# Kernel tuning notes

Hardware: AMD Instinct MI355X
Metric: run time of the kernel (lower is better)

The kernel has to match this reference:

```python
import jax, jax.numpy as jnp
import numpy as np

D = 1024       # d_model
L = 4          # num_layers
T = 2048       # sequence length


def setup_inputs() -> dict:
    key = jax.random.key(0)
    ks = jax.random.split(key, 8)
    lim = 1.0 / np.sqrt(2 * D)              # torch default Linear init bound
    xav = np.sqrt(6.0 / (2 * D + D))        # xavier_uniform for time_a/time_b
    u = lambda k, lo, hi: jax.random.uniform(k, (L, 2 * D, D), jnp.float32, lo, hi)
    return {
        "spatial_states": jax.random.normal(ks[0], (T, D), jnp.float32),
        "re_norm": jnp.float32(0.5),
        "dt_phys": jnp.float32(1.0),
        "re_proj_w": jax.random.uniform(ks[1], (D,), jnp.float32, -1.0, 1.0),  # Linear(1,D) weight, bound=1
        "re_proj_b": jax.random.uniform(ks[2], (D,), jnp.float32, -1.0, 1.0),
        "Wf1": u(ks[3], -lim, lim),
        "bf1": jnp.zeros((L, D), jnp.float32),
        "Wf2": u(ks[4], -lim, lim),
        "bf2": jnp.zeros((L, D), jnp.float32),
        "Wta": u(ks[5], -xav, xav),
        "bta": jnp.zeros((L, D), jnp.float32),
        "Wtb": u(ks[6], -xav, xav),
        "btb": jnp.zeros((L, D), jnp.float32),
    }


def reference(spatial_states, re_norm, dt_phys, re_proj_w, re_proj_b,
              Wf1, bf1, Wf2, bf2, Wta, bta, Wtb, btb):
    d = re_proj_w.shape[0]
    # persistent Re residual bias added to every timestep
    seq = spatial_states + re_norm * re_proj_w + re_proj_b  # [T, D]
    n_layers = Wf1.shape[0]
    for l in range(n_layers):
        # fuse the 4 per-cell linears into one [2D, 4D] GEMV per step
        W = jnp.concatenate([Wf1[l], Wf2[l], Wta[l], Wtb[l]], axis=1)  # [2D, 4D]
        b = jnp.concatenate([bf1[l], bf2[l], bta[l], btb[l]])          # [4D]

        def step(h, x, W=W, b=b):
            xh = jnp.concatenate([x, h])          # [2D]
            z = xh @ W + b                        # [4D]
            f1 = jnp.tanh(z[:d])
            f2 = jnp.tanh(z[d:2 * d])
            gate = jax.nn.sigmoid(-z[2 * d:3 * d] * dt_phys + z[3 * d:])
            h_new = gate * f1 + (1.0 - gate) * f2
            return h_new, h_new

        _, seq = jax.lax.scan(step, jnp.zeros((d,), seq.dtype), seq)
    return seq[-1]  # [D]
```

## Files before the change

kernel.cpp:

```cpp
#include <hip/hip_runtime.h>
#include <cstdint>
#include <cstddef>

#define DD 1024
#define TT 2048
#define NL 4
#define CH 64
#define NCH (TT / CH)
#define NTHR 1024
#define BPL 64
#define PBLK (NL * BPL)
#define GUARD_LIM (1 << 20)

__device__ __forceinline__ float fast_tanh(float x) {
  float e = __expf(2.f * x);
  return 1.f - 2.f / (e + 1.f);
}

__device__ __forceinline__ float4 agent_load16(const float* p) {
  float4 r;
  asm volatile("global_load_dwordx4 %0, %1, off sc1\n\t"
               "s_waitcnt vmcnt(0)"
               : "=v"(r) : "v"(p) : "memory");
  return r;
}
__device__ __forceinline__ unsigned agent_load4(const unsigned* p) {
  unsigned r;
  asm volatile("global_load_dword %0, %1, off sc1\n\t"
               "s_waitcnt vmcnt(0)"
               : "=v"(r) : "v"(p) : "memory");
  return r;
}
__device__ __forceinline__ void agent_store16(float* p, float4 v) {
  unsigned long long lo =
      ((unsigned long long)__float_as_uint(v.y) << 32) | __float_as_uint(v.x);
  unsigned long long hi =
      ((unsigned long long)__float_as_uint(v.w) << 32) | __float_as_uint(v.z);
  __hip_atomic_store((unsigned long long*)p, lo,
                     __ATOMIC_RELAXED, __HIP_MEMORY_SCOPE_AGENT);
  __hip_atomic_store(((unsigned long long*)p) + 1, hi,
                     __ATOMIC_RELAXED, __HIP_MEMORY_SCOPE_AGENT);
}

template <int CTRL>
__device__ __forceinline__ float dpp_add(float x) {
  int y = __builtin_amdgcn_update_dpp(0, __float_as_int(x), CTRL, 0xf, 0xf, true);
  return x + __int_as_float(y);
}
__device__ __forceinline__ float wave_allreduce_add(float x) {
  x = dpp_add<0xB1>(x);
  x = dpp_add<0x4E>(x);
  x = dpp_add<0x141>(x);
  x = dpp_add<0x140>(x);
  x += __shfl_xor(x, 16, 64);
  x += __shfl_xor(x, 32, 64);
  return x;
}

__device__ __forceinline__ bool nan_free4(float4 v) {
  unsigned x0 = __float_as_uint(v.x) & 0x7fffffffu;
  unsigned x1 = __float_as_uint(v.y) & 0x7fffffffu;
  unsigned x2 = __float_as_uint(v.z) & 0x7fffffffu;
  unsigned x3 = __float_as_uint(v.w) & 0x7fffffffu;
  return (x0 <= 0x7f800000u) && (x1 <= 0x7f800000u) &&
         (x2 <= 0x7f800000u) && (x3 <= 0x7f800000u);
}

__global__ __launch_bounds__(1024) void prep_kernel(
    const float* __restrict__ sp, const float* __restrict__ rn_p,
    const float* __restrict__ w, const float* __restrict__ b,
    float* __restrict__ X0) {
  int i = blockIdx.x * blockDim.x + threadIdx.x;
  float rn = rn_p[0];
  int c = i & (DD - 1);
  X0[i] = sp[i] + rn * w[c] + b[c];
}

__global__ __launch_bounds__(NTHR, 4) void persist_kernel(
    const float* __restrict__ X0,
    float* __restrict__ HB,
    unsigned* __restrict__ FLG,
    int R,
    const float* __restrict__ Wf1, const float* __restrict__ Wf2,
    const float* __restrict__ Wta, const float* __restrict__ Wtb,
    const float* __restrict__ bf1, const float* __restrict__ bf2,
    const float* __restrict__ bta, const float* __restrict__ btb,
    const float* __restrict__ dt_p,
    float* __restrict__ out_last)
{
  __shared__ __align__(16) float hbuf[2][DD];
  __shared__ float zxbuf[CH][64];
  __shared__ float Xs[64][68];
  __shared__ float Ws[64][64];
  __shared__ __align__(64) float hq[16];
  __shared__ float lds_pad[6144];

  const int tid = threadIdx.x;
  const int w   = tid >> 6;
  const int ln  = tid & 63;
  const int l   = blockIdx.x >> 6;
  const int grp = blockIdx.x & 63;
  const int col = grp * 16 + w;
  const float dtv = dt_p[0];

  if (tid < 6144) lds_pad[tid] = (float)tid;

  const size_t woff = (size_t)l * 2 * DD * DD;

  float4 wA0, wA1, wA2, wA3, wB0, wB1, wB2, wB3;
  float4 wC0, wC1, wC2, wC3, wD0, wD1, wD2, wD3;
#define LOADW(dst, base, g) do { \
    const float* p_ = (base) + (size_t)(DD + (g) * 256 + ln * 4) * DD + col; \
    dst = make_float4(p_[0], p_[DD], p_[2 * DD], p_[3 * DD]); \
  } while (0)
  {
    const float* W_ = Wf1 + woff;
    LOADW(wA0, W_, 0); LOADW(wA1, W_, 1); LOADW(wA2, W_, 2); LOADW(wA3, W_, 3);
    W_ = Wf2 + woff;
    LOADW(wB0, W_, 0); LOADW(wB1, W_, 1); LOADW(wB2, W_, 2); LOADW(wB3, W_, 3);
    W_ = Wta + woff;
    LOADW(wC0, W_, 0); LOADW(wC1, W_, 1); LOADW(wC2, W_, 2); LOADW(wC3, W_, 3);
    W_ = Wtb + woff;
    LOADW(wD0, W_, 0); LOADW(wD1, W_, 1); LOADW(wD2, W_, 2); LOADW(wD3, W_, 3);
  }
#undef LOADW

  const int p  = ln >> 4;
  const float* Wxp = ((p == 0) ? Wf1 : (p == 1) ? Wf2 : (p == 2) ? Wta : Wtb) + woff;
  const float* bsp = ((p == 0) ? bf1 : (p == 1) ? bf2 : (p == 2) ? bta : btb)
                     + (size_t)l * DD;
  const int colx = grp * 16 + (ln & 15);
  const float biasv = bsp[colx];

  const int rsel = grp & (R - 1);
  const float* hread = HB + (size_t)(l * R + rsel) * TT * DD;
  const unsigned* FLGr = FLG + (size_t)(l * R + rsel) * TT * 64;
  const float* xbase = (l == 0) ? X0 : HB + (size_t)((l - 1) * R + rsel) * TT * DD;

  hbuf[0][tid] = 0.f;
  __syncthreads();

#pragma unroll 1
  for (int c = 0; c < NCH; ++c) {
    if (l > 0) {
      if (tid < 256) {
        const float* gsrc = xbase + (size_t)(c * CH + CH - 1) * DD + tid * 4;
        bool ok = false;
        int tries = 0;
        while (true) {
          if (!ok) ok = nan_free4(agent_load16(gsrc));
          if (__all(ok)) break;
          if (++tries > 2) __builtin_amdgcn_s_sleep(8);
          if (tries > GUARD_LIM) break;
        }
      }
      __syncthreads();
    }

    float acc[4];
#pragma unroll
    for (int i = 0; i < 4; ++i) acc[i] = 0.f;

    const int xrow = tid >> 4;
    const int xq   = (tid & 15) * 4;
    const float* xrowp = xbase + (size_t)(c * CH + xrow) * DD + xq;

#pragma unroll 1
    for (int k0 = 0; k0 < DD; k0 += 64) {
      {
        const float* src = xrowp + k0;
        float4 v = (l == 0) ? *(const float4*)src : agent_load16(src);
        Xs[xq + 0][xrow] = v.x; Xs[xq + 1][xrow] = v.y;
        Xs[xq + 2][xrow] = v.z; Xs[xq + 3][xrow] = v.w;
      }
#pragma unroll
      for (int j = 0; j < 4; ++j)
        Ws[w * 4 + j][ln] = Wxp[(size_t)(k0 + w * 4 + j) * DD + colx];
      __syncthreads();
#pragma unroll 16
      for (int kk = 0; kk < 64; ++kk) {
        float wvk = Ws[kk][ln];
        float4 x = *(const float4*)&Xs[kk][w * 4];
        acc[0] = fmaf(x.x, wvk, acc[0]); acc[1] = fmaf(x.y, wvk, acc[1]);
        acc[2] = fmaf(x.z, wvk, acc[2]); acc[3] = fmaf(x.w, wvk, acc[3]);
      }
      __syncthreads();
    }
#pragma unroll
    for (int i = 0; i < 4; ++i) zxbuf[w * 4 + i][ln] = acc[i] + biasv;
    __syncthreads();

#pragma unroll 1
    for (int tl = 0; tl < CH; ++tl) {
      const int t = c * CH + tl;
      const float* rbuf = hbuf[t & 1];

      float zxv = (ln < 4) ? zxbuf[tl][ln * 16 + w] : 0.f;
      float a0 = (ln == 0) ? zxv : 0.f;
      float a1 = (ln == 1) ? zxv : 0.f;
      float a2 = (ln == 2) ? zxv : 0.f;
      float a3 = (ln == 3) ? zxv : 0.f;

#define DOTG(g, WA, WB, WC, WD) do { \
      float4 h4 = *(const float4*)&rbuf[(g) * 256 + ln * 4]; \
      a0 = fmaf(h4.x, WA.x, a0); a0 = fmaf(h4.y, WA.y, a0); \
      a0 = fmaf(h4.z, WA.z, a0); a0 = fmaf(h4.w, WA.w, a0); \
      a1 = fmaf(h4.x, WB.x, a1); a1 = fmaf(h4.y, WB.y, a1); \
      a1 = fmaf(h4.z, WB.z, a1); a1 = fmaf(h4.w, WB.w, a1); \
      a2 = fmaf(h4.x, WC.x, a2); a2 = fmaf(h4.y, WC.y, a2); \
      a2 = fmaf(h4.z, WC.z, a2); a2 = fmaf(h4.w, WC.w, a2); \
      a3 = fmaf(h4.x, WD.x, a3); a3 = fmaf(h4.y, WD.y, a3); \
      a3 = fmaf(h4.z, WD.z, a3); a3 = fmaf(h4.w, WD.w, a3); \
    } while (0)
      DOTG(0, wA0, wB0, wC0, wD0);
      DOTG(1, wA1, wB1, wC1, wD1);
      DOTG(2, wA2, wB2, wC2, wD2);
      DOTG(3, wA3, wB3, wC3, wD3);
#undef DOTG

      a0 = wave_allreduce_add(a0);
      a1 = wave_allreduce_add(a1);
      a2 = wave_allreduce_add(a2);
      a3 = wave_allreduce_add(a3);

      float f1 = fast_tanh(a0);
      float f2 = fast_tanh(a1);
      float g  = 1.f / (1.f + __expf(a2 * dtv - a3));
      float h  = fmaf(g, f1 - f2, f2);

      if (ln == 0) hq[w] = h;
      if (l == 3 && t == TT - 1 && ln == 0 && out_last) out_last[col] = h;
      __syncthreads();

      if (w == 0 && ln < R) {
        float* dst = HB + (size_t)(l * R + ln) * TT * DD + (size_t)t * DD + grp * 16;
        float4 q0 = *(const float4*)&hq[0];
        float4 q1 = *(const float4*)&hq[4];
        float4 q2 = *(const float4*)&hq[8];
        float4 q3 = *(const float4*)&hq[12];
        agent_store16(dst + 0,  q0);
        agent_store16(dst + 4,  q1);
        agent_store16(dst + 8,  q2);
        agent_store16(dst + 12, q3);
        __hip_atomic_store(&FLG[((size_t)(l * R + ln) * TT + t) * 64 + grp],
                           (unsigned)t, __ATOMIC_RELAXED,
                           __HIP_MEMORY_SCOPE_AGENT);
      }

      if (t < TT - 1 && tid < 256) {
        const unsigned* fp = FLGr + (size_t)t * 64 + ln;
        bool fok = false;
        int tries = 0;
        while (true) {
          if (!fok) fok = (agent_load4(fp) == (unsigned)t);
          if (__all(fok)) break;
          if (++tries > 8) __builtin_amdgcn_s_sleep(1);
          if (tries > GUARD_LIM) break;
        }
        const float* src = &hread[(size_t)t * DD + tid * 4];
        float4 v = agent_load16(src);
        int g2 = 0;
        while (!nan_free4(v)) {
          if (++g2 > GUARD_LIM) { v = make_float4(0.f, 0.f, 0.f, 0.f); break; }
          if (g2 > 4) __builtin_amdgcn_s_sleep(1);
          v = agent_load16(src);
        }
        *(float4*)&hbuf[(t + 1) & 1][tid * 4] = v;
      }
      __syncthreads();
    }
  }

  if ((uintptr_t)out_last == 1) out_last[0] = lds_pad[tid & 1023];
}

extern "C" void kernel_launch(void* const* d_in, const int* in_sizes, int n_in,
                              void* d_out, int out_size, void* d_ws, size_t ws_size,
                              hipStream_t stream) {
  const float* sp  = (const float*)d_in[0];
  const float* rn  = (const float*)d_in[1];
  const float* dt  = (const float*)d_in[2];
  const float* rw  = (const float*)d_in[3];
  const float* rb  = (const float*)d_in[4];
  const float* Wf1 = (const float*)d_in[5];
  const float* bf1 = (const float*)d_in[6];
  const float* Wf2 = (const float*)d_in[7];
  const float* bf2 = (const float*)d_in[8];
  const float* Wta = (const float*)d_in[9];
  const float* bta = (const float*)d_in[10];
  const float* Wtb = (const float*)d_in[11];
  const float* btb = (const float*)d_in[12];

  float* ws = (float*)d_ws;
  float* X0 = ws;
  float* HB = ws + (size_t)TT * DD;
  float* out = (float*)d_out;
  const size_t seqB = sizeof(float) * (size_t)TT * DD;
  const size_t flgPerRep = (size_t)TT * 64 * sizeof(unsigned);

  int R = 1;
  for (int cand = 8; cand >= 1; cand >>= 1) {
    size_t need = seqB + (size_t)NL * cand * (seqB + flgPerRep);
    if (need <= ws_size) { R = cand; break; }
  }
  unsigned* FLG = (unsigned*)(ws + (size_t)(1 + NL * R) * TT * DD);

  (void)hipMemsetAsync(HB, 0xFF, (size_t)NL * R * (seqB + flgPerRep), stream);
  prep_kernel<<<(TT * DD) / 1024, 1024, 0, stream>>>(sp, rn, rw, rb, X0);
  persist_kernel<<<PBLK, NTHR, 0, stream>>>(X0, HB, FLG, R, Wf1, Wf2, Wta, Wtb,
      bf1, bf2, bta, btb, dt, out);
}
```

Measured before the change: 11.01 ms.

## Replace per-step flag array and barrier with NaN-sentinel polling and LDS ready counters

Removes the per-timestep flag array and its polling. Readers now spin directly on the 0xFF (NaN) sentinel in the hidden-state buffer, which drops one dependent global round trip per step. The mid-step __syncthreads is replaced by a workgroup-scope atomic counter that the storing wave waits on, plus per-quarter ready flags so compute waves can begin dot products as each 256-wide slice of h arrives. This relies on the 16-byte store being seen without torn halves (stored as two 64-bit atomics, so all-non-NaN detection per float4 is needed) and adds spin loops inside the workgroup.

```diff
diff --git a/kernel.cpp b/kernel.cpp
--- a/kernel.cpp
+++ b/kernel.cpp
@@ -24,13 +24,6 @@
                : "=v"(r) : "v"(p) : "memory");
   return r;
 }
-__device__ __forceinline__ unsigned agent_load4(const unsigned* p) {
-  unsigned r;
-  asm volatile("global_load_dword %0, %1, off sc1\n\t"
-               "s_waitcnt vmcnt(0)"
-               : "=v"(r) : "v"(p) : "memory");
-  return r;
-}
 __device__ __forceinline__ void agent_store16(float* p, float4 v) {
   unsigned long long lo =
       ((unsigned long long)__float_as_uint(v.y) << 32) | __float_as_uint(v.x);
@@ -79,7 +72,6 @@
 __global__ __launch_bounds__(NTHR, 4) void persist_kernel(
     const float* __restrict__ X0,
     float* __restrict__ HB,
-    unsigned* __restrict__ FLG,
     int R,
     const float* __restrict__ Wf1, const float* __restrict__ Wf2,
     const float* __restrict__ Wta, const float* __restrict__ Wtb,
@@ -93,6 +85,8 @@
   __shared__ float Xs[64][68];
   __shared__ float Ws[64][64];
   __shared__ __align__(64) float hq[16];
+  __shared__ int ready[4];
+  __shared__ int hcnt;
   __shared__ float lds_pad[6144];
 
   const int tid = threadIdx.x;
@@ -104,6 +98,10 @@
   const float dtv = dt_p[0];
 
   if (tid < 6144) lds_pad[tid] = (float)tid;
+  if (tid == 0) {
+    hcnt = 0;
+    ready[0] = ready[1] = ready[2] = ready[3] = -1;
+  }
 
   const size_t woff = (size_t)l * 2 * DD * DD;
 
@@ -134,7 +132,6 @@
 
   const int rsel = grp & (R - 1);
   const float* hread = HB + (size_t)(l * R + rsel) * TT * DD;
-  const unsigned* FLGr = FLG + (size_t)(l * R + rsel) * TT * 64;
   const float* xbase = (l == 0) ? X0 : HB + (size_t)((l - 1) * R + rsel) * TT * DD;
 
   hbuf[0][tid] = 0.f;
@@ -201,6 +198,14 @@
       float a2 = (ln == 2) ? zxv : 0.f;
       float a3 = (ln == 3) ? zxv : 0.f;
 
+#define WAITG(g) do {                                                       \
+      int gd_ = 0;                                                          \
+      while (__hip_atomic_load(&ready[g], __ATOMIC_ACQUIRE,                 \
+                               __HIP_MEMORY_SCOPE_WORKGROUP) < t - 1) {     \
+        if (++gd_ > GUARD_LIM) break;                                       \
+      }                                                                     \
+    } while (0)
+
 #define DOTG(g, WA, WB, WC, WD) do { \
       float4 h4 = *(const float4*)&rbuf[(g) * 256 + ln * 4]; \
       a0 = fmaf(h4.x, WA.x, a0); a0 = fmaf(h4.y, WA.y, a0); \
@@ -212,11 +217,12 @@
       a3 = fmaf(h4.x, WD.x, a3); a3 = fmaf(h4.y, WD.y, a3); \
       a3 = fmaf(h4.z, WD.z, a3); a3 = fmaf(h4.w, WD.w, a3); \
     } while (0)
-      DOTG(0, wA0, wB0, wC0, wD0);
-      DOTG(1, wA1, wB1, wC1, wD1);
-      DOTG(2, wA2, wB2, wC2, wD2);
-      DOTG(3, wA3, wB3, wC3, wD3);
+      WAITG(0); DOTG(0, wA0, wB0, wC0, wD0);
+      WAITG(1); DOTG(1, wA1, wB1, wC1, wD1);
+      WAITG(2); DOTG(2, wA2, wB2, wC2, wD2);
+      WAITG(3); DOTG(3, wA3, wB3, wC3, wD3);
 #undef DOTG
+#undef WAITG
 
       a0 = wave_allreduce_add(a0);
       a1 = wave_allreduce_add(a1);
@@ -228,44 +234,53 @@
       float g  = 1.f / (1.f + __expf(a2 * dtv - a3));
       float h  = fmaf(g, f1 - f2, f2);
 
-      if (ln == 0) hq[w] = h;
+      if (ln == 0) {
+        hq[w] = h;
+        __hip_atomic_fetch_add(&hcnt, 1, __ATOMIC_RELEASE,
+                               __HIP_MEMORY_SCOPE_WORKGROUP);
+      }
       if (l == 3 && t == TT - 1 && ln == 0 && out_last) out_last[col] = h;
-      __syncthreads();
-
-      if (w == 0 && ln < R) {
-        float* dst = HB + (size_t)(l * R + ln) * TT * DD + (size_t)t * DD + grp * 16;
-        float4 q0 = *(const float4*)&hq[0];
-        float4 q1 = *(const float4*)&hq[4];
-        float4 q2 = *(const float4*)&hq[8];
-        float4 q3 = *(const float4*)&hq[12];
-        agent_store16(dst + 0,  q0);
-        agent_store16(dst + 4,  q1);
-        agent_store16(dst + 8,  q2);
-        agent_store16(dst + 12, q3);
-        __hip_atomic_store(&FLG[((size_t)(l * R + ln) * TT + t) * 64 + grp],
-                           (unsigned)t, __ATOMIC_RELAXED,
-                           __HIP_MEMORY_SCOPE_AGENT);
-      }
-
-      if (t < TT - 1 && tid < 256) {
-        const unsigned* fp = FLGr + (size_t)t * 64 + ln;
-        bool fok = false;
+
+      if (w == 15) {
+        const int target = 16 * (t + 1);
+        int gd = 0;
+        while (__hip_atomic_load(&hcnt, __ATOMIC_ACQUIRE,
+                                 __HIP_MEMORY_SCOPE_WORKGROUP) < target) {
+          if (++gd > GUARD_LIM) break;
+        }
+        if (ln < R) {
+          float* dst = HB + (size_t)(l * R + ln) * TT * DD +
+                       (size_t)t * DD + grp * 16;
+          float4 q0 = *(const float4*)&hq[0];
+          float4 q1 = *(const float4*)&hq[4];
+          float4 q2 = *(const float4*)&hq[8];
+          float4 q3 = *(const float4*)&hq[12];
+          agent_store16(dst + 0,  q0);
+          agent_store16(dst + 4,  q1);
+          agent_store16(dst + 8,  q2);
+          agent_store16(dst + 12, q3);
+        }
+      }
+
+      if (t < TT - 1 && w < 4) {
+        const float* src = &hread[(size_t)t * DD + w * 256 + ln * 4];
+        float4 v = make_float4(0.f, 0.f, 0.f, 0.f);
+        bool ok = false;
         int tries = 0;
         while (true) {
-          if (!fok) fok = (agent_load4(fp) == (unsigned)t);
-          if (__all(fok)) break;
+          if (!ok) {
+            v = agent_load16(src);
+            ok = nan_free4(v);
+          }
+          if (__all(ok)) break;
           if (++tries > 8) __builtin_amdgcn_s_sleep(1);
           if (tries > GUARD_LIM) break;
         }
-        const float* src = &hread[(size_t)t * DD + tid * 4];
-        float4 v = agent_load16(src);
-        int g2 = 0;
-        while (!nan_free4(v)) {
-          if (++g2 > GUARD_LIM) { v = make_float4(0.f, 0.f, 0.f, 0.f); break; }
-          if (g2 > 4) __builtin_amdgcn_s_sleep(1);
-          v = agent_load16(src);
-        }
-        *(float4*)&hbuf[(t + 1) & 1][tid * 4] = v;
+        if (!ok) v = make_float4(0.f, 0.f, 0.f, 0.f);
+        *(float4*)&hbuf[(t + 1) & 1][w * 256 + ln * 4] = v;
+        if (ln == 0)
+          __hip_atomic_store(&ready[w], t, __ATOMIC_RELEASE,
+                             __HIP_MEMORY_SCOPE_WORKGROUP);
       }
       __syncthreads();
     }
@@ -296,17 +311,15 @@
   float* HB = ws + (size_t)TT * DD;
   float* out = (float*)d_out;
   const size_t seqB = sizeof(float) * (size_t)TT * DD;
-  const size_t flgPerRep = (size_t)TT * 64 * sizeof(unsigned);
 
   int R = 1;
   for (int cand = 8; cand >= 1; cand >>= 1) {
-    size_t need = seqB + (size_t)NL * cand * (seqB + flgPerRep);
+    size_t need = seqB * (size_t)(1 + NL * cand);
     if (need <= ws_size) { R = cand; break; }
   }
-  unsigned* FLG = (unsigned*)(ws + (size_t)(1 + NL * R) * TT * DD);
-
-  (void)hipMemsetAsync(HB, 0xFF, (size_t)NL * R * (seqB + flgPerRep), stream);
+
+  (void)hipMemsetAsync(HB, 0xFF, (size_t)NL * R * seqB, stream);
   prep_kernel<<<(TT * DD) / 1024, 1024, 0, stream>>>(sp, rn, rw, rb, X0);
-  persist_kernel<<<PBLK, NTHR, 0, stream>>>(X0, HB, FLG, R, Wf1, Wf2, Wta, Wtb,
+  persist_kernel<<<PBLK, NTHR, 0, stream>>>(X0, HB, R, Wf1, Wf2, Wta, Wtb,
       bf1, bf2, bta, btb, dt, out);
 }
```

Result: faster. 10.36 ms (-5.9%).
